# Kernel optimization log

Hardware: AMD Instinct MI355X
Metric: run time of the kernel (lower is better)

Reference implementation:

```python
import jax, jax.numpy as jnp
import numpy as np

B, T, D = 4, 8192, 1024
BLOCKS, TOPK, MACRO, SLOTS = 64, 16, 4, 64
RMS_EPS = 1.1920929e-07  # torch.finfo(float32).eps, F.rms_norm default


def setup_inputs() -> dict:
    key = jax.random.key(0)
    ks = jax.random.split(key, 7)
    return {
        "prev_hidden": jax.random.normal(ks[0], (B, T, D), jnp.float32),
        "prev_nll": jax.random.uniform(ks[1], (B, T), jnp.float32),
        "query": jax.random.normal(ks[2], (SLOTS, D), jnp.float32) * 0.02,
        "W_sum": jax.random.normal(ks[3], (D, 2 * D), jnp.float32) / np.sqrt(2 * D),
        "W_k": jax.random.normal(ks[4], (D, D), jnp.float32) / np.sqrt(D),
        "W_v": jax.random.normal(ks[5], (D, D), jnp.float32) / np.sqrt(D),
        "W_o": jax.random.normal(ks[6], (D, D), jnp.float32) / np.sqrt(D),
    }


def _rms_norm(x):
    return x * jax.lax.rsqrt(jnp.mean(x * x, axis=-1, keepdims=True) + RMS_EPS)


def _zscore(x):
    m = x.mean(axis=1, keepdims=True)
    s = jnp.maximum(x.std(axis=1, keepdims=True), 1e-6)  # unbiased=False
    return (x - m) / s


def reference(prev_hidden, prev_nll, query, W_sum, W_k, W_v, W_o):
    b, t, d = prev_hidden.shape
    # --- micro segments: equal blocks (t divisible by BLOCKS -> linspace edges exact)
    L = t // BLOCKS
    seg = prev_hidden.reshape(b, BLOCKS, L, d)
    seg_mean = seg.mean(axis=2)          # [B, BLOCKS, D]
    seg_last = seg[:, :, -1, :]          # [B, BLOCKS, D]
    hid_score = jnp.linalg.norm(seg_mean, axis=-1)            # [B, BLOCKS]
    sur_score = prev_nll.reshape(b, BLOCKS, L).mean(axis=-1)  # [B, BLOCKS]
    scores = _zscore(hid_score) + _zscore(sur_score)          # utility_source='both'
    idx = jnp.sort(jax.lax.top_k(scores, TOPK)[1], axis=-1)   # [B, TOPK]
    gmean = jnp.take_along_axis(seg_mean, idx[:, :, None], axis=1)
    glast = jnp.take_along_axis(seg_last, idx[:, :, None], axis=1)
    micro = jnp.concatenate([gmean, glast], axis=-1)          # [B, TOPK, 2D]
    # --- hierarchical: macro segments + global
    Lm = t // MACRO
    mseg = prev_hidden.reshape(b, MACRO, Lm, d)
    macro = jnp.concatenate([mseg.mean(axis=2), mseg[:, :, -1, :]], axis=-1)
    glob = jnp.concatenate([prev_hidden.mean(axis=1), prev_hidden[:, -1, :]], axis=-1)[:, None, :]
    feats = jnp.concatenate([micro, macro, glob], axis=1)     # [B, S=21, 2D]
    summaries = _rms_norm(jnp.einsum('bsf,df->bsd', feats, W_sum))
    # --- cross-attention of learned prefix queries over sources
    keys = jnp.einsum('bsd,ed->bse', summaries, W_k)
    vals = jnp.einsum('bsd,ed->bse', summaries, W_v)
    logits = jnp.einsum('qd,bsd->bqs', query, keys) / jnp.sqrt(jnp.float32(d))
    attn = jax.nn.softmax(logits.astype(jnp.float32), axis=-1).astype(summaries.dtype)
    prefix = jnp.einsum('bqs,bse->bqe', attn, vals)
    return jnp.einsum('bqe,oe->bqo', prefix, W_o)
```

## Files before the change

### kernel.cpp

```cpp
#include <hip/hip_runtime.h>
#include <stdint.h>
#include <stddef.h>

#define B_ 4
#define T_ 8192
#define D_ 1024
#define NBLK 64
#define SEGL 128
#define TOPK_ 16
#define NS 21
#define MPAD 96
#define RMS_EPS_ 1.1920929e-07f

typedef float f32x4 __attribute__((ext_vector_type(4)));
typedef __bf16 bf16x8 __attribute__((ext_vector_type(8)));
typedef unsigned short us8 __attribute__((ext_vector_type(8)));

__device__ __forceinline__ unsigned short f2bf(float f) {
    union { float f; unsigned int u; } v; v.f = f;
    unsigned int r = v.u + 0x7FFFu + ((v.u >> 16) & 1u);
    return (unsigned short)(r >> 16);
}
__device__ __forceinline__ float4 ld4(const float* p) { return *(const float4*)p; }

__global__ __launch_bounds__(512) void seg_stats(
        const float* __restrict__ ph, const float* __restrict__ nll,
        float* __restrict__ seg_mean, float* __restrict__ hid, float* __restrict__ sur) {
    int g = blockIdx.x; int b = g >> 6; int blk = g & 63;
    int tid = threadIdx.x; int half = tid >> 8; int c = tid & 255;
    const float* base = ph + ((size_t)b * T_ + blk * SEGL + half * 64) * D_ + 4 * c;
    float ax = 0.f, ay = 0.f, az = 0.f, aw = 0.f;
    #pragma unroll 8
    for (int r = 0; r < 64; r++) {
        float4 v = ld4(base + (size_t)r * D_);
        ax += v.x; ay += v.y; az += v.z; aw += v.w;
    }
    __shared__ float4 tmp[256];
    __shared__ float red[256];
    __shared__ float nl[128];
    if (tid < 128) nl[tid] = nll[b * T_ + blk * SEGL + tid];
    if (half) { float4 t; t.x = ax; t.y = ay; t.z = az; t.w = aw; tmp[c] = t; }
    __syncthreads();
    if (!half) {
        float4 t2 = tmp[c];
        float mx = (ax + t2.x) * (1.f/128.f), my = (ay + t2.y) * (1.f/128.f);
        float mz = (az + t2.z) * (1.f/128.f), mw = (aw + t2.w) * (1.f/128.f);
        float4 m; m.x = mx; m.y = my; m.z = mz; m.w = mw;
        *(float4*)(seg_mean + (size_t)g * D_ + 4 * c) = m;
        red[c] = mx*mx + my*my + mz*mz + mw*mw;
    }
    __syncthreads();
    for (int s2 = 128; s2 > 0; s2 >>= 1) { if (tid < s2) red[tid] += red[tid + s2]; __syncthreads(); }
    for (int s2 = 64;  s2 > 0; s2 >>= 1) { if (tid < s2) nl[tid]  += nl[tid + s2];  __syncthreads(); }
    if (tid == 0) { hid[g] = sqrtf(red[0]); sur[g] = nl[0] * (1.f/128.f); }
}

__global__ __launch_bounds__(256) void feats_build(
        const float* __restrict__ ph, const float* __restrict__ seg_mean,
        const float* __restrict__ hid, const float* __restrict__ sur,
        unsigned short* __restrict__ feats) {
    int r = blockIdx.x; int t = threadIdx.x;
    unsigned short* row0 = feats + (size_t)r * 2048 + 4 * t;
    unsigned short* row1 = row0 + 1024;
    if (r >= B_ * NS) {
        ushort4 z4; z4.x = z4.y = z4.z = z4.w = 0;
        *(ushort4*)row0 = z4; *(ushort4*)row1 = z4;
        return;
    }
    int b = r / NS, s = r % NS;
    __shared__ float sc[64];
    __shared__ int sidx[16];
    if (t < 64) {
        float h = hid[b * NBLK + t];
        float ss0 = sur[b * NBLK + t];
        float mh = h; for (int o = 32; o; o >>= 1) mh += __shfl_xor(mh, o); mh *= (1.f/64.f);
        float dh = h - mh; float vh = dh * dh;
        for (int o = 32; o; o >>= 1) vh += __shfl_xor(vh, o); vh *= (1.f/64.f);
        float sh = fmaxf(sqrtf(vh), 1e-6f);
        float ms = ss0; for (int o = 32; o; o >>= 1) ms += __shfl_xor(ms, o); ms *= (1.f/64.f);
        float ds = ss0 - ms; float vs = ds * ds;
        for (int o = 32; o; o >>= 1) vs += __shfl_xor(vs, o); vs *= (1.f/64.f);
        float ssd = fmaxf(sqrtf(vs), 1e-6f);
        sc[t] = dh / sh + ds / ssd;
    }
    __syncthreads();
    if (t < 64) {
        float z = sc[t];
        int rank = 0;
        for (int j = 0; j < 64; j++) {
            float oj = sc[j];
            rank += (oj > z) || (oj == z && j < t);
        }
        bool sel = rank < TOPK_;
        unsigned long long mask = __ballot(sel);
        int pos = __popcll(mask & ((1ull << t) - 1ull));
        if (sel) sidx[pos] = t;
    }
    __syncthreads();

    float mx = 0, my = 0, mz = 0, mw = 0;
    int lastrow;
    if (s < 16) {
        int blk = sidx[s];
        float4 v = ld4(seg_mean + (size_t)(b * NBLK + blk) * D_ + 4 * t);
        mx = v.x; my = v.y; mz = v.z; mw = v.w;
        lastrow = blk * SEGL + SEGL - 1;
    } else if (s < 20) {
        int m = s - 16;
        for (int j = 0; j < 16; j++) {
            float4 v = ld4(seg_mean + (size_t)(b * NBLK + m * 16 + j) * D_ + 4 * t);
            mx += v.x; my += v.y; mz += v.z; mw += v.w;
        }
        mx *= (1.f/16.f); my *= (1.f/16.f); mz *= (1.f/16.f); mw *= (1.f/16.f);
        lastrow = m * 2048 + 2047;
    } else {
        for (int j = 0; j < 64; j++) {
            float4 v = ld4(seg_mean + (size_t)(b * NBLK + j) * D_ + 4 * t);
            mx += v.x; my += v.y; mz += v.z; mw += v.w;
        }
        mx *= (1.f/64.f); my *= (1.f/64.f); mz *= (1.f/64.f); mw *= (1.f/64.f);
        lastrow = T_ - 1;
    }
    float4 lv = ld4(ph + ((size_t)b * T_ + lastrow) * D_ + 4 * t);
    ushort4 hm; hm.x = f2bf(mx); hm.y = f2bf(my); hm.z = f2bf(mz); hm.w = f2bf(mw);
    ushort4 hl; hl.x = f2bf(lv.x); hl.y = f2bf(lv.y); hl.z = f2bf(lv.z); hl.w = f2bf(lv.w);
    *(ushort4*)row0 = hm;
    *(ushort4*)row1 = hl;
}

template<int K, int MODE>
__global__ __launch_bounds__(512) void gemm_v3(
        const void* __restrict__ Av,
        const float* __restrict__ B0, const float* __restrict__ B1,
        float* __restrict__ C0f, unsigned short* __restrict__ C0b,
        float* __restrict__ C1f, unsigned short* __restrict__ C1b,
        float* __restrict__ sumsq) {
    constexpr int KW = K / 8;
    constexpr int NSTEP = KW / 32;
    const float* Bw = (MODE == 2 && blockIdx.y) ? B1 : B0;
    float* Cf          = (MODE == 2 && blockIdx.y) ? C1f : C0f;
    unsigned short* Cb = (MODE == 2 && blockIdx.y) ? C1b : C0b;

    int n0 = blockIdx.x * 16;
    int tid = threadIdx.x, wave = tid >> 6, lane = tid & 63;
    int quad = lane >> 4, l16 = lane & 15;
    int kbase = wave * KW;

    f32x4 acc[6];
    #pragma unroll
    for (int i = 0; i < 6; i++) acc[i] = (f32x4){0.f, 0.f, 0.f, 0.f};

    float scl[6];
    if (MODE == 2) {
        #pragma unroll
        for (int mi = 0; mi < 6; mi++)
            scl[mi] = rsqrtf(sumsq[mi * 16 + l16] * (1.f/1024.f) + RMS_EPS_);
    }

    const float* bp = Bw + (size_t)(n0 + l16) * K + kbase + quad * 8;

    #pragma unroll 4
    for (int s = 0; s < NSTEP; s++) {
        float4 b0 = ld4(bp + s * 32);
        float4 b1 = ld4(bp + s * 32 + 4);
        us8 braw;
        braw[0] = f2bf(b0.x); braw[1] = f2bf(b0.y); braw[2] = f2bf(b0.z); braw[3] = f2bf(b0.w);
        braw[4] = f2bf(b1.x); braw[5] = f2bf(b1.y); braw[6] = f2bf(b1.z); braw[7] = f2bf(b1.w);
        bf16x8 bfr = __builtin_bit_cast(bf16x8, braw);
        #pragma unroll
        for (int mi = 0; mi < 6; mi++) {
            bf16x8 af;
            if (MODE == 2) {
                const float* apf = (const float*)Av + (size_t)(mi * 16 + l16) * K + kbase + quad * 8 + s * 32;
                float4 a0 = ld4(apf), a1 = ld4(apf + 4);
                us8 ar;
                ar[0] = f2bf(a0.x * scl[mi]); ar[1] = f2bf(a0.y * scl[mi]);
                ar[2] = f2bf(a0.z * scl[mi]); ar[3] = f2bf(a0.w * scl[mi]);
                ar[4] = f2bf(a1.x * scl[mi]); ar[5] = f2bf(a1.y * scl[mi]);
                ar[6] = f2bf(a1.z * scl[mi]); ar[7] = f2bf(a1.w * scl[mi]);
                af = __builtin_bit_cast(bf16x8, ar);
            } else {
                af = __builtin_bit_cast(bf16x8,
                    *(const us8*)((const unsigned short*)Av + (size_t)(mi * 16 + l16) * K + kbase + quad * 8 + s * 32));
            }
            acc[mi] = __builtin_amdgcn_mfma_f32_16x16x32_bf16(af, bfr, acc[mi], 0, 0, 0);
        }
    }

    __shared__ float part[8][6][16][16];
    #pragma unroll
    for (int mi = 0; mi < 6; mi++)
        #pragma unroll
        for (int r = 0; r < 4; r++)
            part[wave][mi][quad * 4 + r][l16] = acc[mi][r];
    __syncthreads();

    #pragma unroll
    for (int j = 0; j < 3; j++) {
        int o = tid + j * 512;
        int mi = o >> 8, rr = (o >> 4) & 15, cc = o & 15;
        float v = 0.f;
        #pragma unroll
        for (int w = 0; w < 8; w++) v += part[w][mi][rr][cc];
        int row = mi * 16 + rr, col = n0 + cc;
        if (MODE == 1) {
            float v2 = v * v;
            #pragma unroll
            for (int off = 1; off < 16; off <<= 1) v2 += __shfl_xor(v2, off);
            if ((tid & 15) == 0) atomicAdd(&sumsq[row], v2);
        }
        if (Cf) Cf[(size_t)row * 1024 + col] = v;
        if (Cb) Cb[(size_t)row * 1024 + col] = f2bf(v);
    }
}

__global__ __launch_bounds__(256) void attn_out(
        const float* __restrict__ query, const float* __restrict__ keys,
        const float* __restrict__ valsO, float* __restrict__ out) {
    int g = blockIdx.x; int b = g >> 6; int q = g & 63;
    int tid = threadIdx.x, wave = tid >> 6, lane = tid & 63;
    __shared__ float attnw[24];
    const float* qrow = query + (size_t)q * D_ + lane * 16;
    float4 qv0 = ld4(qrow), qv1 = ld4(qrow + 4), qv2 = ld4(qrow + 8), qv3 = ld4(qrow + 12);
    for (int s = wave; s < NS; s += 4) {
        const float* krow = keys + (size_t)(b * NS + s) * D_ + lane * 16;
        float4 k0 = ld4(krow), k1 = ld4(krow + 4), k2 = ld4(krow + 8), k3 = ld4(krow + 12);
        float a = qv0.x*k0.x + qv0.y*k0.y + qv0.z*k0.z + qv0.w*k0.w
                + qv1.x*k1.x + qv1.y*k1.y + qv1.z*k1.z + qv1.w*k1.w
                + qv2.x*k2.x + qv2.y*k2.y + qv2.z*k2.z + qv2.w*k2.w
                + qv3.x*k3.x + qv3.y*k3.y + qv3.z*k3.z + qv3.w*k3.w;
        for (int o = 32; o; o >>= 1) a += __shfl_xor(a, o);
        if (lane == 0) attnw[s] = a * 0.03125f;
    }
    __syncthreads();
    if (tid == 0) {
        float mx = -1e30f;
        for (int s = 0; s < NS; s++) mx = fmaxf(mx, attnw[s]);
        float sum = 0.f;
        for (int s = 0; s < NS; s++) { float e = expf(attnw[s] - mx); attnw[s] = e; sum += e; }
        float inv = 1.f / sum;
        for (int s = 0; s < NS; s++) attnw[s] *= inv;
    }
    __syncthreads();
    float ax = 0, ay = 0, az = 0, aw = 0;
    #pragma unroll
    for (int s = 0; s < NS; s++) {
        float w = attnw[s];
        float4 v = ld4(valsO + (size_t)(b * NS + s) * D_ + 4 * tid);
        ax += w * v.x; ay += w * v.y; az += w * v.z; aw += w * v.w;
    }
    float4 o4; o4.x = ax; o4.y = ay; o4.z = az; o4.w = aw;
    *(float4*)(out + (size_t)g * D_ + 4 * tid) = o4;
}

extern "C" void kernel_launch(void* const* d_in, const int* in_sizes, int n_in,
                              void* d_out, int out_size, void* d_ws, size_t ws_size,
                              hipStream_t stream) {
    (void)in_sizes; (void)n_in; (void)out_size; (void)ws_size;
    const float* ph    = (const float*)d_in[0];
    const float* nll   = (const float*)d_in[1];
    const float* query = (const float*)d_in[2];
    const float* W_sum = (const float*)d_in[3];
    const float* W_k   = (const float*)d_in[4];
    const float* W_v   = (const float*)d_in[5];
    const float* W_o   = (const float*)d_in[6];
    float* out = (float*)d_out;

    char* ws = (char*)d_ws;
    float*          seg_mean = (float*)(ws + 0);
    float*          hid      = (float*)(ws + 1048576);
    float*          sur      = (float*)(ws + 1049600);
    float*          sumsq    = (float*)(ws + 1050624);
    unsigned short* feats    = (unsigned short*)(ws + 1051136);
    float*          presum_f = (float*)(ws + 1444352);
    float*          keys_f   = (float*)(ws + 1837568);
    unsigned short* vals_b   = (unsigned short*)(ws + 2230784);
    float*          valsO_f  = (float*)(ws + 2427392);

    hipMemsetAsync(sumsq, 0, MPAD * sizeof(float), stream);
    seg_stats<<<B_ * NBLK, 512, 0, stream>>>(ph, nll, seg_mean, hid, sur);
    feats_build<<<MPAD, 256, 0, stream>>>(ph, seg_mean, hid, sur, feats);
    gemm_v3<2048, 1><<<dim3(64, 1), 512, 0, stream>>>(
        feats, W_sum, nullptr, presum_f, nullptr, nullptr, nullptr, sumsq);
    gemm_v3<1024, 2><<<dim3(64, 2), 512, 0, stream>>>(
        presum_f, W_k, W_v, keys_f, nullptr, nullptr, vals_b, sumsq);
    gemm_v3<1024, 0><<<dim3(64, 1), 512, 0, stream>>>(
        vals_b, W_o, nullptr, valsO_f, nullptr, nullptr, nullptr, nullptr);
    attn_out<<<B_ * NBLK, 256, 0, stream>>>(query, keys_f, valsO_f, out);
}
```

Baseline: 272.7 us.

## Split-K GEMMs with LDS-staged tiles and a separate RMSNorm pass

```diff
diff --git a/kernel.cpp b/kernel.cpp
--- a/kernel.cpp
+++ b/kernel.cpp
@@ -11,6 +11,7 @@
 #define NS 21
 #define MPAD 96
 #define RMS_EPS_ 1.1920929e-07f
+#define PART 98304
 
 typedef float f32x4 __attribute__((ext_vector_type(4)));
 typedef __bf16 bf16x8 __attribute__((ext_vector_type(8)));
@@ -128,103 +129,136 @@
     *(ushort4*)row1 = hl;
 }
 
-template<int K, int MODE>
-__global__ __launch_bounds__(512) void gemm_v3(
+template<int K, int AMODE>
+__global__ __launch_bounds__(512) void gemm_lds(
         const void* __restrict__ Av,
         const float* __restrict__ B0, const float* __restrict__ B1,
-        float* __restrict__ C0f, unsigned short* __restrict__ C0b,
-        float* __restrict__ C1f, unsigned short* __restrict__ C1b,
-        float* __restrict__ sumsq) {
-    constexpr int KW = K / 8;
-    constexpr int NSTEP = KW / 32;
-    const float* Bw = (MODE == 2 && blockIdx.y) ? B1 : B0;
-    float* Cf          = (MODE == 2 && blockIdx.y) ? C1f : C0f;
-    unsigned short* Cb = (MODE == 2 && blockIdx.y) ? C1b : C0b;
-
-    int n0 = blockIdx.x * 16;
+        float* __restrict__ C0, float* __restrict__ C1) {
+    const float* Bw = blockIdx.z ? B1 : B0;
+    float* Cp       = blockIdx.z ? C1 : C0;
+    int n0 = blockIdx.x * 64;
+    int kc = blockIdx.y;
+    Cp += (size_t)kc * PART;
     int tid = threadIdx.x, wave = tid >> 6, lane = tid & 63;
     int quad = lane >> 4, l16 = lane & 15;
-    int kbase = wave * KW;
-
+
+    __shared__ unsigned short Bs[64 * 264];
+    __shared__ unsigned short As[96 * 264];
+
+    #pragma unroll
+    for (int i = 0; i < 4; i++) {
+        int id = tid + 512 * i;
+        int r = id >> 5, c = id & 31;
+        const float* src = Bw + (size_t)(n0 + r) * K + kc * 256 + c * 8;
+        float4 v0 = ld4(src), v1 = ld4(src + 4);
+        us8 h;
+        h[0] = f2bf(v0.x); h[1] = f2bf(v0.y); h[2] = f2bf(v0.z); h[3] = f2bf(v0.w);
+        h[4] = f2bf(v1.x); h[5] = f2bf(v1.y); h[6] = f2bf(v1.z); h[7] = f2bf(v1.w);
+        *(us8*)&Bs[r * 264 + c * 8] = h;
+    }
+    #pragma unroll
+    for (int i = 0; i < 6; i++) {
+        int id = tid + 512 * i;
+        int r = id >> 5, c = id & 31;
+        if (AMODE == 0) {
+            const unsigned short* A = (const unsigned short*)Av;
+            *(us8*)&As[r * 264 + c * 8] =
+                *(const us8*)(A + (size_t)r * K + kc * 256 + c * 8);
+        } else {
+            const float* A = (const float*)Av;
+            const float* s0 = A + (size_t)r * 1024 + kc * 256 + c * 8;
+            float4 a0 = ld4(s0), a1 = ld4(s0 + 4);
+            #pragma unroll
+            for (int p = 1; p < 4; p++) {
+                float4 b0 = ld4(s0 + p * PART), b1 = ld4(s0 + p * PART + 4);
+                a0.x += b0.x; a0.y += b0.y; a0.z += b0.z; a0.w += b0.w;
+                a1.x += b1.x; a1.y += b1.y; a1.z += b1.z; a1.w += b1.w;
+            }
+            us8 h;
+            h[0] = f2bf(a0.x); h[1] = f2bf(a0.y); h[2] = f2bf(a0.z); h[3] = f2bf(a0.w);
+            h[4] = f2bf(a1.x); h[5] = f2bf(a1.y); h[6] = f2bf(a1.z); h[7] = f2bf(a1.w);
+            *(us8*)&As[r * 264 + c * 8] = h;
+        }
+    }
+    __syncthreads();
+
+    int strip = wave >> 1, kh = wave & 1;
     f32x4 acc[6];
     #pragma unroll
     for (int i = 0; i < 6; i++) acc[i] = (f32x4){0.f, 0.f, 0.f, 0.f};
-
-    float scl[6];
-    if (MODE == 2) {
+    const unsigned short* bbase = &Bs[(strip * 16 + l16) * 264 + kh * 128 + quad * 8];
+    const unsigned short* abase = &As[l16 * 264 + kh * 128 + quad * 8];
+    #pragma unroll
+    for (int kk = 0; kk < 128; kk += 32) {
+        bf16x8 bfr = __builtin_bit_cast(bf16x8, *(const us8*)(bbase + kk));
+        #pragma unroll
+        for (int mi = 0; mi < 6; mi++) {
+            bf16x8 af = __builtin_bit_cast(bf16x8, *(const us8*)(abase + mi * 16 * 264 + kk));
+            acc[mi] = __builtin_amdgcn_mfma_f32_16x16x32_bf16(af, bfr, acc[mi], 0, 0, 0);
+        }
+    }
+    __syncthreads();
+
+    float* scr = (float*)As;
+    if (kh == 1) {
         #pragma unroll
         for (int mi = 0; mi < 6; mi++)
-            scl[mi] = rsqrtf(sumsq[mi * 16 + l16] * (1.f/1024.f) + RMS_EPS_);
-    }
-
-    const float* bp = Bw + (size_t)(n0 + l16) * K + kbase + quad * 8;
-
-    #pragma unroll 4
-    for (int s = 0; s < NSTEP; s++) {
-        float4 b0 = ld4(bp + s * 32);
-        float4 b1 = ld4(bp + s * 32 + 4);
-        us8 braw;
-        braw[0] = f2bf(b0.x); braw[1] = f2bf(b0.y); braw[2] = f2bf(b0.z); braw[3] = f2bf(b0.w);
-        braw[4] = f2bf(b1.x); braw[5] = f2bf(b1.y); braw[6] = f2bf(b1.z); braw[7] = f2bf(b1.w);
-        bf16x8 bfr = __builtin_bit_cast(bf16x8, braw);
-        #pragma unroll
-        for (int mi = 0; mi < 6; mi++) {
-            bf16x8 af;
-            if (MODE == 2) {
-                const float* apf = (const float*)Av + (size_t)(mi * 16 + l16) * K + kbase + quad * 8 + s * 32;
-                float4 a0 = ld4(apf), a1 = ld4(apf + 4);
-                us8 ar;
-                ar[0] = f2bf(a0.x * scl[mi]); ar[1] = f2bf(a0.y * scl[mi]);
-                ar[2] = f2bf(a0.z * scl[mi]); ar[3] = f2bf(a0.w * scl[mi]);
-                ar[4] = f2bf(a1.x * scl[mi]); ar[5] = f2bf(a1.y * scl[mi]);
-                ar[6] = f2bf(a1.z * scl[mi]); ar[7] = f2bf(a1.w * scl[mi]);
-                af = __builtin_bit_cast(bf16x8, ar);
-            } else {
-                af = __builtin_bit_cast(bf16x8,
-                    *(const us8*)((const unsigned short*)Av + (size_t)(mi * 16 + l16) * K + kbase + quad * 8 + s * 32));
+            #pragma unroll
+            for (int r = 0; r < 4; r++)
+                scr[((strip * 6 + mi) * 16 + quad * 4 + r) * 16 + l16] = acc[mi][r];
+    }
+    __syncthreads();
+    if (kh == 0) {
+        #pragma unroll
+        for (int mi = 0; mi < 6; mi++)
+            #pragma unroll
+            for (int r = 0; r < 4; r++) {
+                float v = acc[mi][r] + scr[((strip * 6 + mi) * 16 + quad * 4 + r) * 16 + l16];
+                Cp[(size_t)(mi * 16 + quad * 4 + r) * 1024 + n0 + strip * 16 + l16] = v;
             }
-            acc[mi] = __builtin_amdgcn_mfma_f32_16x16x32_bf16(af, bfr, acc[mi], 0, 0, 0);
-        }
-    }
-
-    __shared__ float part[8][6][16][16];
-    #pragma unroll
-    for (int mi = 0; mi < 6; mi++)
-        #pragma unroll
-        for (int r = 0; r < 4; r++)
-            part[wave][mi][quad * 4 + r][l16] = acc[mi][r];
-    __syncthreads();
-
-    #pragma unroll
-    for (int j = 0; j < 3; j++) {
-        int o = tid + j * 512;
-        int mi = o >> 8, rr = (o >> 4) & 15, cc = o & 15;
-        float v = 0.f;
-        #pragma unroll
-        for (int w = 0; w < 8; w++) v += part[w][mi][rr][cc];
-        int row = mi * 16 + rr, col = n0 + cc;
-        if (MODE == 1) {
-            float v2 = v * v;
-            #pragma unroll
-            for (int off = 1; off < 16; off <<= 1) v2 += __shfl_xor(v2, off);
-            if ((tid & 15) == 0) atomicAdd(&sumsq[row], v2);
-        }
-        if (Cf) Cf[(size_t)row * 1024 + col] = v;
-        if (Cb) Cb[(size_t)row * 1024 + col] = f2bf(v);
-    }
+    }
+}
+
+__global__ __launch_bounds__(256) void rmsnorm8(
+        const float* __restrict__ pp, unsigned short* __restrict__ y) {
+    int r = blockIdx.x; int t = threadIdx.x;
+    float4 v = (float4){0.f, 0.f, 0.f, 0.f};
+    #pragma unroll
+    for (int c = 0; c < 8; c++) {
+        float4 u = ld4(pp + (size_t)c * PART + (size_t)r * D_ + 4 * t);
+        v.x += u.x; v.y += u.y; v.z += u.z; v.w += u.w;
+    }
+    __shared__ float red[256];
+    red[t] = v.x*v.x + v.y*v.y + v.z*v.z + v.w*v.w;
+    __syncthreads();
+    for (int s2 = 128; s2 > 0; s2 >>= 1) { if (t < s2) red[t] += red[t + s2]; __syncthreads(); }
+    float scale = rsqrtf(red[0] * (1.f/1024.f) + RMS_EPS_);
+    ushort4 h;
+    h.x = f2bf(v.x * scale); h.y = f2bf(v.y * scale);
+    h.z = f2bf(v.z * scale); h.w = f2bf(v.w * scale);
+    *(ushort4*)(y + (size_t)r * D_ + 4 * t) = h;
 }
 
 __global__ __launch_bounds__(256) void attn_out(
-        const float* __restrict__ query, const float* __restrict__ keys,
-        const float* __restrict__ valsO, float* __restrict__ out) {
+        const float* __restrict__ query, const float* __restrict__ keys_p,
+        const float* __restrict__ valsO_p, float* __restrict__ out) {
     int g = blockIdx.x; int b = g >> 6; int q = g & 63;
     int tid = threadIdx.x, wave = tid >> 6, lane = tid & 63;
     __shared__ float attnw[24];
     const float* qrow = query + (size_t)q * D_ + lane * 16;
     float4 qv0 = ld4(qrow), qv1 = ld4(qrow + 4), qv2 = ld4(qrow + 8), qv3 = ld4(qrow + 12);
     for (int s = wave; s < NS; s += 4) {
-        const float* krow = keys + (size_t)(b * NS + s) * D_ + lane * 16;
-        float4 k0 = ld4(krow), k1 = ld4(krow + 4), k2 = ld4(krow + 8), k3 = ld4(krow + 12);
+        const float* krow = keys_p + (size_t)(b * NS + s) * D_ + lane * 16;
+        float4 k0 = (float4){0,0,0,0}, k1 = k0, k2 = k0, k3 = k0;
+        #pragma unroll
+        for (int c = 0; c < 4; c++) {
+            const float* kp = krow + (size_t)c * PART;
+            float4 u0 = ld4(kp), u1 = ld4(kp + 4), u2 = ld4(kp + 8), u3 = ld4(kp + 12);
+            k0.x += u0.x; k0.y += u0.y; k0.z += u0.z; k0.w += u0.w;
+            k1.x += u1.x; k1.y += u1.y; k1.z += u1.z; k1.w += u1.w;
+            k2.x += u2.x; k2.y += u2.y; k2.z += u2.z; k2.w += u2.w;
+            k3.x += u3.x; k3.y += u3.y; k3.z += u3.z; k3.w += u3.w;
+        }
         float a = qv0.x*k0.x + qv0.y*k0.y + qv0.z*k0.z + qv0.w*k0.w
                 + qv1.x*k1.x + qv1.y*k1.y + qv1.z*k1.z + qv1.w*k1.w
                 + qv2.x*k2.x + qv2.y*k2.y + qv2.z*k2.z + qv2.w*k2.w
@@ -246,7 +280,12 @@
     #pragma unroll
     for (int s = 0; s < NS; s++) {
         float w = attnw[s];
-        float4 v = ld4(valsO + (size_t)(b * NS + s) * D_ + 4 * tid);
+        float4 v = (float4){0,0,0,0};
+        #pragma unroll
+        for (int c = 0; c < 4; c++) {
+            float4 u = ld4(valsO_p + (size_t)c * PART + (size_t)(b * NS + s) * D_ + 4 * tid);
+            v.x += u.x; v.y += u.y; v.z += u.z; v.w += u.w;
+        }
         ax += w * v.x; ay += w * v.y; az += w * v.z; aw += w * v.w;
     }
     float4 o4; o4.x = ax; o4.y = ay; o4.z = az; o4.w = aw;
@@ -270,21 +309,21 @@
     float*          seg_mean = (float*)(ws + 0);
     float*          hid      = (float*)(ws + 1048576);
     float*          sur      = (float*)(ws + 1049600);
-    float*          sumsq    = (float*)(ws + 1050624);
-    unsigned short* feats    = (unsigned short*)(ws + 1051136);
-    float*          presum_f = (float*)(ws + 1444352);
-    float*          keys_f   = (float*)(ws + 1837568);
-    unsigned short* vals_b   = (unsigned short*)(ws + 2230784);
-    float*          valsO_f  = (float*)(ws + 2427392);
-
-    hipMemsetAsync(sumsq, 0, MPAD * sizeof(float), stream);
+    unsigned short* feats    = (unsigned short*)(ws + 1050624);
+    float*          presum_p = (float*)(ws + 1443840);
+    unsigned short* summ_b   = (unsigned short*)(ws + 4589568);
+    float*          keys_p   = (float*)(ws + 4786176);
+    float*          vals_p   = (float*)(ws + 6359040);
+    float*          valsO_p  = (float*)(ws + 7931904);
+
     seg_stats<<<B_ * NBLK, 512, 0, stream>>>(ph, nll, seg_mean, hid, sur);
     feats_build<<<MPAD, 256, 0, stream>>>(ph, seg_mean, hid, sur, feats);
-    gemm_v3<2048, 1><<<dim3(64, 1), 512, 0, stream>>>(
-        feats, W_sum, nullptr, presum_f, nullptr, nullptr, nullptr, sumsq);
-    gemm_v3<1024, 2><<<dim3(64, 2), 512, 0, stream>>>(
-        presum_f, W_k, W_v, keys_f, nullptr, nullptr, vals_b, sumsq);
-    gemm_v3<1024, 0><<<dim3(64, 1), 512, 0, stream>>>(
-        vals_b, W_o, nullptr, valsO_f, nullptr, nullptr, nullptr, nullptr);
-    attn_out<<<B_ * NBLK, 256, 0, stream>>>(query, keys_f, valsO_f, out);
-}
+    gemm_lds<2048, 0><<<dim3(16, 8, 1), 512, 0, stream>>>(
+        feats, W_sum, nullptr, presum_p, nullptr);
+    rmsnorm8<<<MPAD, 256, 0, stream>>>(presum_p, summ_b);
+    gemm_lds<1024, 0><<<dim3(16, 4, 2), 512, 0, stream>>>(
+        summ_b, W_k, W_v, keys_p, vals_p);
+    gemm_lds<1024, 1><<<dim3(16, 4, 1), 512, 0, stream>>>(
+        vals_p, W_o, nullptr, valsO_p, nullptr);
+    attn_out<<<B_ * NBLK, 256, 0, stream>>>(query, keys_p, valsO_p, out);
+}
```

New measurement: 256.4 us. 1.06x faster.
